# Kernel tuning notes

Hardware: AMD Instinct MI355X
Metric: run time of the kernel (lower is better)

The kernel has to match this reference:

```python
import jax, jax.numpy as jnp
import numpy as np
import math

B, S, IN_DIM, FEATURES = 4, 4096, 1024, 1024


def setup_inputs() -> dict:
    key = jax.random.key(0)
    kx, kk = jax.random.split(key)
    x = jax.random.normal(kx, (B, S, IN_DIM), dtype=jnp.float32)
    # bool kernel representing a +1/-1 binary weight matrix
    kernel = jax.random.randint(kk, (IN_DIM, FEATURES), 0, 2).astype(jnp.bool_)
    scale = jnp.float32(1.0 / math.sqrt(IN_DIM))  # nn.initializers.constant(1/sqrt(in_dim))
    return {"x": x, "kernel": kernel, "scale": scale}


def reference(x, kernel, scale):
    # conn_dense: bool kernel encodes +1 (True) / -1 (False) weights
    w = jnp.where(kernel, 1.0, -1.0).astype(x.dtype)  # [in_dim, features]
    # [b, s, in] @ [in, f] -> [b, s, f], then scalar scale
    return scale * jnp.einsum("bsi,if->bsf", x, w)
```

## Files before the change

### kernel.cpp

```cpp
#include <hip/hip_runtime.h>


#define M_TOT 16384
#define N_TOT 1024
#define K_TOT 1024

typedef __attribute__((ext_vector_type(8))) short bf16x8;
typedef __attribute__((ext_vector_type(4))) float f32x4;

__device__ __forceinline__ unsigned short f2bf(float f) {
    unsigned int u = __builtin_bit_cast(unsigned int, f);
    u += 0x7FFFu + ((u >> 16) & 1u);
    return (unsigned short)(u >> 16);
}

__global__ void detect_mode(const unsigned int* __restrict__ k32, int* __restrict__ flag) {
    __shared__ int s;
    if (threadIdx.x == 0) s = 0;
    __syncthreads();
    int bad = 0;
    for (int i = threadIdx.x; i < 1024; i += 256)
        if (k32[i] > 1u) bad = 1;
    if (bad) atomicOr(&s, 1);
    __syncthreads();
    if (threadIdx.x == 0) flag[0] = s;
}

__global__ __launch_bounds__(256) void convert_x(
    const float4* __restrict__ x, ushort4* __restrict__ xb)
{
    const int S = gridDim.x * blockDim.x;
    int g = blockIdx.x * blockDim.x + threadIdx.x;
    #pragma unroll
    for (int j = 0; j < 4; ++j) {
        int idx = g + j * S;
        float4 v = x[idx];
        ushort4 h;
        h.x = f2bf(v.x); h.y = f2bf(v.y); h.z = f2bf(v.z); h.w = f2bf(v.w);
        xb[idx] = h;
    }
}

__global__ __launch_bounds__(256) void convert_w(
    const void* __restrict__ w_raw, unsigned short* __restrict__ wt,
    const int* __restrict__ mode_p)
{
    __shared__ unsigned short tile[64 * 72];
    const int tid = threadIdx.x;
    const int k0 = (blockIdx.x & 15) * 64;
    const int n0 = (blockIdx.x >> 4) * 64;
    const int row = tid >> 2;
    const int seg = (tid & 3) * 16;

    if (mode_p[0] == 0) {
        const unsigned int* w = (const unsigned int*)w_raw;
        const uint4* src = reinterpret_cast<const uint4*>(
            w + (size_t)(k0 + row) * N_TOT + n0 + seg);
        #pragma unroll
        for (int q = 0; q < 4; ++q) {
            uint4 v = src[q];
            ushort4 h;
            h.x = v.x ? 0x3F80u : 0xBF80u;
            h.y = v.y ? 0x3F80u : 0xBF80u;
            h.z = v.z ? 0x3F80u : 0xBF80u;
            h.w = v.w ? 0x3F80u : 0xBF80u;
            *reinterpret_cast<ushort4*>(&tile[row * 72 + seg + q * 4]) = h;
        }
    } else {
        const unsigned char* w = (const unsigned char*)w_raw;
        uint4 v = *reinterpret_cast<const uint4*>(
            w + (size_t)(k0 + row) * N_TOT + n0 + seg);
        unsigned char b[16];
        *reinterpret_cast<uint4*>(b) = v;
        #pragma unroll
        for (int q = 0; q < 4; ++q) {
            ushort4 h;
            h.x = b[q * 4 + 0] ? 0x3F80u : 0xBF80u;
            h.y = b[q * 4 + 1] ? 0x3F80u : 0xBF80u;
            h.z = b[q * 4 + 2] ? 0x3F80u : 0xBF80u;
            h.w = b[q * 4 + 3] ? 0x3F80u : 0xBF80u;
            *reinterpret_cast<ushort4*>(&tile[row * 72 + seg + q * 4]) = h;
        }
    }
    __syncthreads();
    {
        int n = tid >> 2, kseg = (tid & 3) * 16;
        ushort4 o[4];
        #pragma unroll
        for (int j = 0; j < 16; ++j)
            ((unsigned short*)o)[j] = tile[(kseg + j) * 72 + n];
        ushort4* dst = reinterpret_cast<ushort4*>(wt + (size_t)(n0 + n) * K_TOT + k0 + kseg);
        dst[0] = o[0]; dst[1] = o[1]; dst[2] = o[2]; dst[3] = o[3];
    }
}

__global__ __launch_bounds__(256) void bf16_gemm(
    const unsigned short* __restrict__ A,
    const unsigned short* __restrict__ BT,
    const float* __restrict__ scale_p, float* __restrict__ out)
{
    __shared__ unsigned short As[128 * 64];
    __shared__ unsigned short Bs[128 * 64];

    const int tid  = threadIdx.x;
    const int lane = tid & 63;
    const int wave = tid >> 6;
    const int wm = (wave & 1) * 64;
    const int wn = (wave >> 1) * 64;

    const int j  = blockIdx.x & 7;
    const int s  = blockIdx.x >> 3;
    const int by = ((s >> 3) << 3) | j;
    const int bx = s & 7;
    const int m0 = by * 128, n0 = bx * 128;

    const int fr = lane & 15, fq = lane >> 4;
    const float scale = scale_p[0];

    const int srow = wave * 32 + (lane >> 3);
    const int skch = (lane & 7) ^ (lane >> 3);

    f32x4 acc[4][4] = {};

    for (int k0 = 0; k0 < K_TOT; k0 += 64) {
        #pragma unroll
        for (int q = 0; q < 4; ++q) {
            const unsigned short* g = A + (size_t)(m0 + srow + q * 8) * K_TOT + k0 + skch * 8;
            __builtin_amdgcn_global_load_lds(
                (const __attribute__((address_space(1))) void*)g,
                (__attribute__((address_space(3))) void*)&As[wave * 2048 + q * 512],
                16, 0, 0);
        }
        #pragma unroll
        for (int q = 0; q < 4; ++q) {
            const unsigned short* g = BT + (size_t)(n0 + srow + q * 8) * K_TOT + k0 + skch * 8;
            __builtin_amdgcn_global_load_lds(
                (const __attribute__((address_space(1))) void*)g,
                (__attribute__((address_space(3))) void*)&Bs[wave * 2048 + q * 512],
                16, 0, 0);
        }
        __syncthreads();

        #pragma unroll
        for (int ks = 0; ks < 2; ++ks) {
            bf16x8 af[4], bfr[4];
            #pragma unroll
            for (int mi = 0; mi < 4; ++mi) {
                int r  = wm + mi * 16 + fr;
                int ch = (ks * 4 + fq) ^ (r & 7);
                af[mi] = *reinterpret_cast<const bf16x8*>(&As[r * 64 + ch * 8]);
            }
            #pragma unroll
            for (int ni = 0; ni < 4; ++ni) {
                int r  = wn + ni * 16 + fr;
                int ch = (ks * 4 + fq) ^ (r & 7);
                bfr[ni] = *reinterpret_cast<const bf16x8*>(&Bs[r * 64 + ch * 8]);
            }
            #pragma unroll
            for (int mi = 0; mi < 4; ++mi)
                #pragma unroll
                for (int ni = 0; ni < 4; ++ni)
                    acc[mi][ni] = __builtin_amdgcn_mfma_f32_16x16x32_bf16(
                        af[mi], bfr[ni], acc[mi][ni], 0, 0, 0);
        }
        __syncthreads();
    }

    #pragma unroll
    for (int mi = 0; mi < 4; ++mi) {
        #pragma unroll
        for (int ni = 0; ni < 4; ++ni) {
            const int col  = n0 + wn + ni * 16 + fr;
            const int rowb = m0 + wm + mi * 16 + fq * 4;
            #pragma unroll
            for (int jj = 0; jj < 4; ++jj)
                out[(size_t)(rowb + jj) * N_TOT + col] = scale * acc[mi][ni][jj];
        }
    }
}

#define BKP 40
__global__ __launch_bounds__(256, 2) void binary_dense_gemm(
    const float* __restrict__ x, const int* __restrict__ kern,
    const float* __restrict__ scale_p, float* __restrict__ out)
{
    __shared__ unsigned short Asf[128 * BKP];
    __shared__ unsigned short Bsf[128 * BKP];
    const int tid = threadIdx.x, lane = tid & 63, wave = tid >> 6;
    const int wm = (wave & 1) * 64, wn = (wave >> 1) * 64;
    const int bx = blockIdx.x & 7, by = blockIdx.x >> 3;
    const int m0 = by * 128, n0 = bx * 128;
    const float scale = scale_p[0];
    const int fr = lane & 15, fq = lane >> 4;
    f32x4 acc[4][4] = {};
    for (int k0 = 0; k0 < K_TOT; k0 += 32) {
        #pragma unroll
        for (int i = 0; i < 4; ++i) {
            int slot = tid + i * 256, row = slot >> 3, kg = (slot & 7) << 2;
            const float4 v = *reinterpret_cast<const float4*>(x + (size_t)(m0 + row) * K_TOT + k0 + kg);
            ushort4 h;
            h.x = f2bf(v.x); h.y = f2bf(v.y); h.z = f2bf(v.z); h.w = f2bf(v.w);
            *reinterpret_cast<ushort4*>(&Asf[row * BKP + kg]) = h;
        }
        #pragma unroll
        for (int i = 0; i < 4; ++i) {
            int slot = tid + i * 256, nl = slot & 127, kg = (slot >> 7) << 2;
            ushort4 h;
            h.x = kern[(size_t)(k0 + kg + 0) * N_TOT + n0 + nl] ? 0x3F80u : 0xBF80u;
            h.y = kern[(size_t)(k0 + kg + 1) * N_TOT + n0 + nl] ? 0x3F80u : 0xBF80u;
            h.z = kern[(size_t)(k0 + kg + 2) * N_TOT + n0 + nl] ? 0x3F80u : 0xBF80u;
            h.w = kern[(size_t)(k0 + kg + 3) * N_TOT + n0 + nl] ? 0x3F80u : 0xBF80u;
            *reinterpret_cast<ushort4*>(&Bsf[nl * BKP + kg]) = h;
        }
        __syncthreads();
        bf16x8 af[4], bfr[4];
        #pragma unroll
        for (int mi = 0; mi < 4; ++mi)
            af[mi] = *reinterpret_cast<const bf16x8*>(&Asf[(wm + mi * 16 + fr) * BKP + fq * 8]);
        #pragma unroll
        for (int ni = 0; ni < 4; ++ni)
            bfr[ni] = *reinterpret_cast<const bf16x8*>(&Bsf[(wn + ni * 16 + fr) * BKP + fq * 8]);
        #pragma unroll
        for (int mi = 0; mi < 4; ++mi)
            #pragma unroll
            for (int ni = 0; ni < 4; ++ni)
                acc[mi][ni] = __builtin_amdgcn_mfma_f32_16x16x32_bf16(af[mi], bfr[ni], acc[mi][ni], 0, 0, 0);
        __syncthreads();
    }
    #pragma unroll
    for (int mi = 0; mi < 4; ++mi)
        #pragma unroll
        for (int ni = 0; ni < 4; ++ni) {
            const int col = n0 + wn + ni * 16 + fr;
            const int rowb = m0 + wm + mi * 16 + fq * 4;
            #pragma unroll
            for (int jj = 0; jj < 4; ++jj)
                out[(size_t)(rowb + jj) * N_TOT + col] = scale * acc[mi][ni][jj];
        }
}

extern "C" void kernel_launch(void* const* d_in, const int* in_sizes, int n_in,
                              void* d_out, int out_size, void* d_ws, size_t ws_size,
                              hipStream_t stream) {
    const float* x     = (const float*)d_in[0];
    const void*  kern  = d_in[1];
    const float* scale = (const float*)d_in[2];
    float*       out   = (float*)d_out;

    const size_t xb_bytes = (size_t)M_TOT * K_TOT * 2;
    const size_t wt_bytes = (size_t)N_TOT * K_TOT * 2;
    const size_t flag_off = 256;
    if (ws_size >= flag_off + xb_bytes + wt_bytes) {
        int*            flag = (int*)d_ws;
        unsigned short* xb   = (unsigned short*)((char*)d_ws + flag_off);
        unsigned short* wt   = (unsigned short*)((char*)d_ws + flag_off + xb_bytes);
        hipLaunchKernelGGL(detect_mode, dim3(1), dim3(256), 0, stream,
                           (const unsigned int*)kern, flag);
        hipLaunchKernelGGL(convert_w, dim3(256), dim3(256), 0, stream, kern, wt, flag);
        hipLaunchKernelGGL(convert_x, dim3(4096), dim3(256), 0, stream,
                           (const float4*)x, (ushort4*)xb);
        hipLaunchKernelGGL(bf16_gemm, dim3(1024), dim3(256), 0, stream,
                           xb, wt, scale, out);
    } else {
        hipLaunchKernelGGL(binary_dense_gemm, dim3(1024), dim3(256), 0, stream,
                           x, (const int*)kern, scale, out);
    }
}
```

Measured before the change: 161.8 us.

## Fuse fp32-to-bf16 conversion of X into the GEMM's A-tile load

Drops the separate convert_x pass and its 32 MB bf16 workspace. The GEMM now reads fp32 X straight from global memory, converts pairs with the packed v_cvt_pk_bf16_f32 instruction, and writes swizzled bf16 into LDS. This removes one kernel launch plus the write and re-read of the bf16 copy of X. In exchange, the A loads become synchronous register round-trips rather than async global_load_lds, and each A tile is re-read from fp32 by the 8 column blocks. A launch-bounds occupancy hint is also added.

```diff
diff --git a/kernel.cpp b/kernel.cpp
--- a/kernel.cpp
+++ b/kernel.cpp
@@ -12,6 +12,12 @@
     unsigned int u = __builtin_bit_cast(unsigned int, f);
     u += 0x7FFFu + ((u >> 16) & 1u);
     return (unsigned short)(u >> 16);
+}
+
+__device__ __forceinline__ unsigned int cvt_pk_bf16(float lo, float hi) {
+    unsigned int r;
+    asm("v_cvt_pk_bf16_f32 %0, %1, %2" : "=v"(r) : "v"(lo), "v"(hi));
+    return r;
 }
 
 __global__ void detect_mode(const unsigned int* __restrict__ k32, int* __restrict__ flag) {
@@ -26,21 +32,6 @@
     if (threadIdx.x == 0) flag[0] = s;
 }
 
-__global__ __launch_bounds__(256) void convert_x(
-    const float4* __restrict__ x, ushort4* __restrict__ xb)
-{
-    const int S = gridDim.x * blockDim.x;
-    int g = blockIdx.x * blockDim.x + threadIdx.x;
-    #pragma unroll
-    for (int j = 0; j < 4; ++j) {
-        int idx = g + j * S;
-        float4 v = x[idx];
-        ushort4 h;
-        h.x = f2bf(v.x); h.y = f2bf(v.y); h.z = f2bf(v.z); h.w = f2bf(v.w);
-        xb[idx] = h;
-    }
-}
-
 __global__ __launch_bounds__(256) void convert_w(
     const void* __restrict__ w_raw, unsigned short* __restrict__ wt,
     const int* __restrict__ mode_p)
@@ -94,8 +85,8 @@
     }
 }
 
-__global__ __launch_bounds__(256) void bf16_gemm(
-    const unsigned short* __restrict__ A,
+__global__ __launch_bounds__(256, 4) void fused_gemm(
+    const float* __restrict__ X,
     const unsigned short* __restrict__ BT,
     const float* __restrict__ scale_p, float* __restrict__ out)
 {
@@ -117,27 +108,36 @@
     const int fr = lane & 15, fq = lane >> 4;
     const float scale = scale_p[0];
 
-    const int srow = wave * 32 + (lane >> 3);
-    const int skch = (lane & 7) ^ (lane >> 3);
+    const int srow_l = lane >> 3;
+    const int gch    = lane & 7;
+    const int lch    = gch ^ srow_l;
+    const int skch   = gch ^ srow_l;
 
     f32x4 acc[4][4] = {};
 
     for (int k0 = 0; k0 < K_TOT; k0 += 64) {
         #pragma unroll
         for (int q = 0; q < 4; ++q) {
-            const unsigned short* g = A + (size_t)(m0 + srow + q * 8) * K_TOT + k0 + skch * 8;
-            __builtin_amdgcn_global_load_lds(
-                (const __attribute__((address_space(1))) void*)g,
-                (__attribute__((address_space(3))) void*)&As[wave * 2048 + q * 512],
-                16, 0, 0);
-        }
-        #pragma unroll
-        for (int q = 0; q < 4; ++q) {
-            const unsigned short* g = BT + (size_t)(n0 + srow + q * 8) * K_TOT + k0 + skch * 8;
+            const unsigned short* g = BT + (size_t)(n0 + wave * 32 + q * 8 + srow_l) * K_TOT
+                                         + k0 + skch * 8;
             __builtin_amdgcn_global_load_lds(
                 (const __attribute__((address_space(1))) void*)g,
                 (__attribute__((address_space(3))) void*)&Bs[wave * 2048 + q * 512],
                 16, 0, 0);
+        }
+        #pragma unroll
+        for (int q = 0; q < 4; ++q) {
+            const int r = wave * 32 + q * 8 + srow_l;
+            const float4* g = reinterpret_cast<const float4*>(
+                X + (size_t)(m0 + r) * K_TOT + k0 + gch * 8);
+            float4 va = g[0];
+            float4 vb = g[1];
+            uint4 p;
+            p.x = cvt_pk_bf16(va.x, va.y);
+            p.y = cvt_pk_bf16(va.z, va.w);
+            p.z = cvt_pk_bf16(vb.x, vb.y);
+            p.w = cvt_pk_bf16(vb.z, vb.w);
+            *reinterpret_cast<uint4*>(&As[r * 64 + lch * 8]) = p;
         }
         __syncthreads();
 
@@ -247,20 +247,16 @@
     const float* scale = (const float*)d_in[2];
     float*       out   = (float*)d_out;
 
-    const size_t xb_bytes = (size_t)M_TOT * K_TOT * 2;
     const size_t wt_bytes = (size_t)N_TOT * K_TOT * 2;
     const size_t flag_off = 256;
-    if (ws_size >= flag_off + xb_bytes + wt_bytes) {
+    if (ws_size >= flag_off + wt_bytes) {
         int*            flag = (int*)d_ws;
-        unsigned short* xb   = (unsigned short*)((char*)d_ws + flag_off);
-        unsigned short* wt   = (unsigned short*)((char*)d_ws + flag_off + xb_bytes);
+        unsigned short* wt   = (unsigned short*)((char*)d_ws + flag_off);
         hipLaunchKernelGGL(detect_mode, dim3(1), dim3(256), 0, stream,
                            (const unsigned int*)kern, flag);
         hipLaunchKernelGGL(convert_w, dim3(256), dim3(256), 0, stream, kern, wt, flag);
-        hipLaunchKernelGGL(convert_x, dim3(4096), dim3(256), 0, stream,
-                           (const float4*)x, (ushort4*)xb);
-        hipLaunchKernelGGL(bf16_gemm, dim3(1024), dim3(256), 0, stream,
-                           xb, wt, scale, out);
+        hipLaunchKernelGGL(fused_gemm, dim3(1024), dim3(256), 0, stream,
+                           x, wt, scale, out);
     } else {
         hipLaunchKernelGGL(binary_dense_gemm, dim3(1024), dim3(256), 0, stream,
                            x, (const int*)kern, scale, out);
```

Measured after the change: 185.3 us. +14.6%, slower.
